# Optimization experiments

Hardware: AMD Instinct MI355X
Metric: run time of the kernel (lower is better)

## Reference

```python
import jax, jax.numpy as jnp
import numpy as np

N = 100000   # nodes
E = 1600000  # edges (before self loops)
B = 64       # graphs in batch
F_IN = 128
H1, C1 = 8, 8   # conv1: heads=8, per-head channels=8 -> concat out 64
H2, C2 = 1, 8   # conv2: heads=1, out=8, concat=False


def gat_conv(x, src, dst, W, att_src, att_dst, bias, H, C, concat, n_nodes):
    """PyG GATConv (shared src/dst weight, leaky_relu slope 0.2, segment softmax).
    src/dst already include self loops. x: [N, F], W: [F, H*C],
    att_src/att_dst: [1, H, C], bias: [H*C] or [C]."""
    xh = (x @ W).reshape(n_nodes, H, C)                      # [N, H, C]
    a_src = jnp.sum(xh * att_src, axis=-1)                   # [N, H]
    a_dst = jnp.sum(xh * att_dst, axis=-1)                   # [N, H]
    alpha = jax.nn.leaky_relu(a_src[src] + a_dst[dst], 0.2)  # [E', H]
    # numerically stable segment softmax over incoming edges of each dst node
    amax = jax.ops.segment_max(jax.lax.stop_gradient(alpha), dst, num_segments=n_nodes)
    ex = jnp.exp(alpha - amax[dst])
    denom = jax.ops.segment_sum(ex, dst, num_segments=n_nodes)
    alpha = ex / (denom[dst] + 1e-16)                        # [E', H]
    msg = xh[src] * alpha[..., None]                         # [E', H, C]
    out = jax.ops.segment_sum(msg, dst, num_segments=n_nodes)  # [N, H, C]
    out = out.reshape(n_nodes, H * C) if concat else out.mean(axis=1)
    return out + bias


def setup_inputs() -> dict:
    key = jax.random.key(0)
    ks = jax.random.split(key, 12)
    x = jax.random.normal(ks[0], (N, F_IN), dtype=jnp.float32)
    edge_index = jax.random.randint(ks[1], (2, E), 0, N, dtype=jnp.int32)
    batch = jnp.sort(jax.random.randint(ks[2], (N,), 0, B, dtype=jnp.int32))
    g = 0.1
    W1 = jax.random.normal(ks[3], (F_IN, H1 * C1), dtype=jnp.float32) * g
    a1_src = jax.random.normal(ks[4], (1, H1, C1), dtype=jnp.float32) * g
    a1_dst = jax.random.normal(ks[5], (1, H1, C1), dtype=jnp.float32) * g
    b1 = jnp.zeros((H1 * C1,), dtype=jnp.float32)
    W2 = jax.random.normal(ks[6], (H1 * C1, H2 * C2), dtype=jnp.float32) * g
    a2_src = jax.random.normal(ks[7], (1, H2, C2), dtype=jnp.float32) * g
    a2_dst = jax.random.normal(ks[8], (1, H2, C2), dtype=jnp.float32) * g
    b2 = jnp.zeros((C2,), dtype=jnp.float32)
    return {"x": x, "edge_index": edge_index, "batch": batch,
            "W1": W1, "a1_src": a1_src, "a1_dst": a1_dst, "b1": b1,
            "W2": W2, "a2_src": a2_src, "a2_dst": a2_dst, "b2": b2}


def reference(x, edge_index, batch, W1, a1_src, a1_dst, b1, W2, a2_src, a2_dst, b2):
    # add self loops (PyG GATConv default)
    loop = jnp.arange(N, dtype=edge_index.dtype)
    src = jnp.concatenate([edge_index[0], loop])
    dst = jnp.concatenate([edge_index[1], loop])
    # eval mode: dropouts are identity
    h = gat_conv(x, src, dst, W1, a1_src, a1_dst, b1, H1, C1, True, N)
    h = jax.nn.elu(h)
    h = gat_conv(h, src, dst, W2, a2_src, a2_dst, b2, H2, C2, False, N)
    # global mean pool over graphs
    sums = jax.ops.segment_sum(h, batch, num_segments=B)          # [B, C2]
    cnt = jax.ops.segment_sum(jnp.ones((N,), h.dtype), batch, num_segments=B)
    return sums / jnp.maximum(cnt, 1.0)[:, None]
```

## Files before the change

kernel.cpp:

```cpp
#include <hip/hip_runtime.h>
#include <hip/hip_bf16.h>

#define BIN_SHIFT 8
#define BIN_NODES 256
#define BIN_CAP   8192
#define EPT       16

typedef float v2f __attribute__((ext_vector_type(2)));

__device__ __forceinline__ float leaky02(float a) { return fmaxf(a, 0.2f * a); }
__device__ __forceinline__ unsigned short f2bf(float f) {
    __hip_bfloat16 h = __float2bfloat16(f);
    return *(unsigned short*)&h;
}
__device__ __forceinline__ float bflo(unsigned u) { return __uint_as_float(u << 16); }
__device__ __forceinline__ float bfhi(unsigned u) { return __uint_as_float(u & 0xffff0000u); }
__device__ __forceinline__ v2f bf2(unsigned u) {
    v2f r; r.x = __uint_as_float(u << 16); r.y = __uint_as_float(u & 0xffff0000u); return r;
}

__global__ __launch_bounds__(512) void gemm1_att_kernel(const float* __restrict__ x,
                                                        const float* __restrict__ W,
                                                        const float* __restrict__ a1s,
                                                        const float* __restrict__ a1d,
                                                        __hip_bfloat16* __restrict__ xh,
                                                        float* __restrict__ asrc,
                                                        float* __restrict__ adst, int N) {
    __shared__ float ws[128 * 64];
    __shared__ float xs[64][132];
    int tid = threadIdx.x;
    for (int i = tid; i < 2048; i += 512) ((float4*)ws)[i] = ((const float4*)W)[i];
    int row0 = blockIdx.x * 64;
    for (int i = tid; i < 64 * 32; i += 512) {
        int r = i >> 5, c4 = i & 31;
        int row = row0 + r;
        float4 v = make_float4(0.f, 0.f, 0.f, 0.f);
        if (row < N) v = ((const float4*)x)[row * 32 + c4];
        float* p = &xs[r][c4 * 4];
        p[0] = v.x; p[1] = v.y; p[2] = v.z; p[3] = v.w;
    }
    __syncthreads();
    int tc = tid & 15, tr = tid >> 4;
    float acc[2][4] = {};
#pragma unroll 4
    for (int k = 0; k < 128; ++k) {
        float a0 = xs[tr * 2][k];
        float a1 = xs[tr * 2 + 1][k];
        float4 b = *(const float4*)&ws[k * 64 + tc * 4];
        acc[0][0] += a0 * b.x; acc[0][1] += a0 * b.y; acc[0][2] += a0 * b.z; acc[0][3] += a0 * b.w;
        acc[1][0] += a1 * b.x; acc[1][1] += a1 * b.y; acc[1][2] += a1 * b.z; acc[1][3] += a1 * b.w;
    }
    float4 sv = ((const float4*)a1s)[tc];
    float4 dv = ((const float4*)a1d)[tc];
    int head = tc >> 1;
#pragma unroll
    for (int r = 0; r < 2; ++r) {
        int row = row0 + tr * 2 + r;
        if (row < N) {
            uint2 o;
            o.x = (unsigned)f2bf(acc[r][0]) | ((unsigned)f2bf(acc[r][1]) << 16);
            o.y = (unsigned)f2bf(acc[r][2]) | ((unsigned)f2bf(acc[r][3]) << 16);
            *(uint2*)(xh + (size_t)row * 64 + tc * 4) = o;
        }
        float sp = acc[r][0] * sv.x + acc[r][1] * sv.y + acc[r][2] * sv.z + acc[r][3] * sv.w;
        float dp = acc[r][0] * dv.x + acc[r][1] * dv.y + acc[r][2] * dv.z + acc[r][3] * dv.w;
        sp += __shfl_xor(sp, 1);
        dp += __shfl_xor(dp, 1);
        if (!(tc & 1) && row < N) {
            asrc[row * 8 + head] = sp;
            adst[row * 8 + head] = dp;
        }
    }
}

__global__ __launch_bounds__(256) void binB_kernel(const int* __restrict__ ei,
                                                   int* __restrict__ cur,
                                                   unsigned* __restrict__ binned,
                                                   int E, int Etot, int NB) {
    __shared__ int bcnt[512];
    int tid = threadIdx.x;
    for (int i = tid; i < 512; i += 256) bcnt[i] = 0;
    __syncthreads();
    long long base = (long long)blockIdx.x * 256 * EPT;
#pragma unroll 4
    for (int i = 0; i < EPT; ++i) {
        long long e = base + i * 256 + tid;
        if (e < Etot) {
            int dst = (e < E) ? ei[E + e] : (int)(e - E);
            atomicAdd(&bcnt[dst >> BIN_SHIFT], 1);
        }
    }
    __syncthreads();
    for (int b = tid; b < NB; b += 256) {
        int c = bcnt[b];
        bcnt[b] = c ? atomicAdd(&cur[b], c) : 0;
    }
    __syncthreads();
#pragma unroll 4
    for (int i = 0; i < EPT; ++i) {
        long long e = base + i * 256 + tid;
        if (e < Etot) {
            int src, dst;
            if (e < E) { src = ei[e]; dst = ei[E + e]; }
            else       { src = dst = (int)(e - E); }
            int bin = dst >> BIN_SHIFT;
            int p = atomicAdd(&bcnt[bin], 1);
            if (p < BIN_CAP)
                binned[(size_t)bin * BIN_CAP + p] = ((unsigned)(dst & (BIN_NODES - 1)) << 24) | (unsigned)src;
        }
    }
}

__global__ __launch_bounds__(256) void binC_kernel(const int* __restrict__ cur,
                                                   const unsigned* __restrict__ binned,
                                                   int* __restrict__ rowptr,
                                                   int* __restrict__ esrc,
                                                   int N, int Etot, int NB) {
    int bin = blockIdx.x;
    int tid = threadIdx.x;
    __shared__ int psum[256];
    __shared__ int sc[256];
    __shared__ int ndc[256];
    int s = 0;
    for (int i = tid; i < bin; i += 256) s += cur[i];
    psum[tid] = s;
    __syncthreads();
    for (int off = 128; off > 0; off >>= 1) {
        if (tid < off) psum[tid] += psum[tid + off];
        __syncthreads();
    }
    int bbase = psum[0];
    int cnt = cur[bin];
    ndc[tid] = 0;
    __syncthreads();
    const unsigned* bp = binned + (size_t)bin * BIN_CAP;
    for (int i = tid; i < cnt; i += 256)
        atomicAdd(&ndc[bp[i] >> 24], 1);
    __syncthreads();
    int v = ndc[tid];
    sc[tid] = v;
    __syncthreads();
    for (int off = 1; off < 256; off <<= 1) {
        int t = (tid >= off) ? sc[tid - off] : 0;
        __syncthreads();
        sc[tid] += t;
        __syncthreads();
    }
    int excl = sc[tid] - v;
    int node = bin * BIN_NODES + tid;
    if (node < N) rowptr[node] = bbase + excl;
    if (bin == NB - 1 && tid == 0) rowptr[N] = Etot;
    ndc[tid] = excl;
    __syncthreads();
    for (int i = tid; i < cnt; i += 256) {
        unsigned w = bp[i];
        int p = atomicAdd(&ndc[w >> 24], 1);
        esrc[bbase + p] = (int)(w & 0xFFFFFFu);
    }
}

__global__ __launch_bounds__(256) void agg1_kernel(const int* __restrict__ rowptr,
                                                   const int* __restrict__ esrc,
                                                   const float* __restrict__ asrc,
                                                   const float* __restrict__ adst,
                                                   const __hip_bfloat16* __restrict__ xh,
                                                   const float* __restrict__ b1,
                                                   __hip_bfloat16* __restrict__ h1, int N) {
    int node = blockIdx.x * 4 + (threadIdx.x >> 6);
    if (node >= N) return;
    int lane = threadIdx.x & 63;
    unsigned slot = (unsigned)(lane >> 3), h = (unsigned)(lane & 7);
    float adh = adst[(unsigned)node * 8u + h];
    unsigned start = (unsigned)rowptr[node];
    int len = rowptr[node + 1] - (int)start;
    const uint4* xh4 = (const uint4*)xh;
    float d = 0.f;
    v2f acc0 = {0.f, 0.f}, acc1 = {0.f, 0.f}, acc2 = {0.f, 0.f}, acc3 = {0.f, 0.f};
    for (int kb = 0; kb < len; kb += 32) {
        int k0 = kb + (int)slot;
        bool ok0 = k0 < len, ok1 = k0 + 8 < len, ok2 = k0 + 16 < len, ok3 = k0 + 24 < len;
        unsigned s0 = ok0 ? (unsigned)esrc[start + k0] : 0u;
        unsigned s1 = ok1 ? (unsigned)esrc[start + k0 + 8] : 0u;
        unsigned s2 = ok2 ? (unsigned)esrc[start + k0 + 16] : 0u;
        unsigned s3 = ok3 ? (unsigned)esrc[start + k0 + 24] : 0u;
        float a0 = ok0 ? asrc[s0 * 8u + h] : -1e30f;
        float a1 = ok1 ? asrc[s1 * 8u + h] : -1e30f;
        float a2 = ok2 ? asrc[s2 * 8u + h] : -1e30f;
        float a3 = ok3 ? asrc[s3 * 8u + h] : -1e30f;
        uint4 u0 = xh4[s0 * 8u + h];
        uint4 u1 = xh4[s1 * 8u + h];
        uint4 u2 = xh4[s2 * 8u + h];
        uint4 u3 = xh4[s3 * 8u + h];
        float p0 = __expf(leaky02(a0 + adh));
        float p1 = __expf(leaky02(a1 + adh));
        float p2 = __expf(leaky02(a2 + adh));
        float p3 = __expf(leaky02(a3 + adh));
        d += (p0 + p1) + (p2 + p3);
        acc0 += bf2(u0.x) * p0; acc1 += bf2(u0.y) * p0;
        acc2 += bf2(u0.z) * p0; acc3 += bf2(u0.w) * p0;
        acc0 += bf2(u1.x) * p1; acc1 += bf2(u1.y) * p1;
        acc2 += bf2(u1.z) * p1; acc3 += bf2(u1.w) * p1;
        acc0 += bf2(u2.x) * p2; acc1 += bf2(u2.y) * p2;
        acc2 += bf2(u2.z) * p2; acc3 += bf2(u2.w) * p2;
        acc0 += bf2(u3.x) * p3; acc1 += bf2(u3.y) * p3;
        acc2 += bf2(u3.z) * p3; acc3 += bf2(u3.w) * p3;
    }
#pragma unroll
    for (int off = 8; off < 64; off <<= 1) {
        d += __shfl_xor(d, off);
        acc0.x += __shfl_xor(acc0.x, off); acc0.y += __shfl_xor(acc0.y, off);
        acc1.x += __shfl_xor(acc1.x, off); acc1.y += __shfl_xor(acc1.y, off);
        acc2.x += __shfl_xor(acc2.x, off); acc2.y += __shfl_xor(acc2.y, off);
        acc3.x += __shfl_xor(acc3.x, off); acc3.y += __shfl_xor(acc3.y, off);
    }
    float vals[8] = {acc0.x, acc0.y, acc1.x, acc1.y, acc2.x, acc2.y, acc3.x, acc3.y};
    float hv = vals[0];
#pragma unroll
    for (int c = 1; c < 8; ++c) hv = ((int)slot == c) ? vals[c] : hv;
    int f = (int)(h * 8u + slot);
    hv = hv / (d + 1e-16f) + b1[f];
    hv = hv > 0.f ? hv : __expf(hv) - 1.0f;
    float hvp = __shfl(hv, ((lane & 7) << 3) | (lane >> 3));
    h1[(unsigned)node * 64u + (unsigned)lane] = __float2bfloat16(hvp);
}

__global__ __launch_bounds__(256) void gemm2h_kernel(const __hip_bfloat16* __restrict__ h1,
                                                     const float* __restrict__ W2,
                                                     const float* __restrict__ a2s,
                                                     const float* __restrict__ a2d,
                                                     __hip_bfloat16* __restrict__ xh2,
                                                     float* __restrict__ asrc2,
                                                     float* __restrict__ adst2, int N) {
    __shared__ float w2s[512];
    __shared__ float aa[16];
    int tid = threadIdx.x;
    for (int i = tid; i < 512; i += 256) w2s[i] = W2[i];
    if (tid < 8) aa[tid] = a2s[tid];
    else if (tid < 16) aa[tid] = a2d[tid - 8];
    __syncthreads();
    unsigned n = blockIdx.x * 256u + (unsigned)tid;
    if (n >= (unsigned)N) return;
    const uint4* hp = (const uint4*)h1 + n * 8u;
    float q[8] = {};
#pragma unroll
    for (int j = 0; j < 8; ++j) {
        uint4 u = hp[j];
        float hv[8] = {bflo(u.x), bfhi(u.x), bflo(u.y), bfhi(u.y),
                       bflo(u.z), bfhi(u.z), bflo(u.w), bfhi(u.w)};
#pragma unroll
        for (int e = 0; e < 8; ++e) {
            int f = j * 8 + e;
            float4 wa = *(const float4*)&w2s[f * 8];
            float4 wb = *(const float4*)&w2s[f * 8 + 4];
            q[0] += hv[e] * wa.x; q[1] += hv[e] * wa.y;
            q[2] += hv[e] * wa.z; q[3] += hv[e] * wa.w;
            q[4] += hv[e] * wb.x; q[5] += hv[e] * wb.y;
            q[6] += hv[e] * wb.z; q[7] += hv[e] * wb.w;
        }
    }
    uint4 o;
    o.x = (unsigned)f2bf(q[0]) | ((unsigned)f2bf(q[1]) << 16);
    o.y = (unsigned)f2bf(q[2]) | ((unsigned)f2bf(q[3]) << 16);
    o.z = (unsigned)f2bf(q[4]) | ((unsigned)f2bf(q[5]) << 16);
    o.w = (unsigned)f2bf(q[6]) | ((unsigned)f2bf(q[7]) << 16);
    *((uint4*)xh2 + n) = o;
    float s2 = 0.f, d2 = 0.f;
#pragma unroll
    for (int c = 0; c < 8; ++c) { s2 += q[c] * aa[c]; d2 += q[c] * aa[8 + c]; }
    asrc2[n] = s2;
    adst2[n] = d2;
}

__global__ __launch_bounds__(256) void agg2_pool_kernel(const int* __restrict__ rowptr,
                                                        const int* __restrict__ esrc,
                                                        const float* __restrict__ asrc2,
                                                        const float* __restrict__ adst2,
                                                        const __hip_bfloat16* __restrict__ xh2,
                                                        const float* __restrict__ b2,
                                                        const int* __restrict__ batch,
                                                        float* __restrict__ pool,
                                                        float* __restrict__ cnt, int N, int B) {
    __shared__ float ps[64 * 8];
    __shared__ float cs[64];
    int tid = threadIdx.x;
    for (int i = tid; i < 512; i += 256) ps[i] = 0.f;
    if (tid < 64) cs[tid] = 0.f;
    __syncthreads();
    int node = blockIdx.x * 32 + (tid >> 3);
    int slot = tid & 7;
    if (node < N) {
        float adh = adst2[node];
        unsigned start = (unsigned)rowptr[node];
        int len = rowptr[node + 1] - (int)start;
        const uint4* x4 = (const uint4*)xh2;
        float d = 0.f;
        v2f acc0 = {0.f, 0.f}, acc1 = {0.f, 0.f}, acc2 = {0.f, 0.f}, acc3 = {0.f, 0.f};
        for (int kb = 0; kb < len; kb += 32) {
            int k0 = kb + slot;
            bool ok0 = k0 < len, ok1 = k0 + 8 < len, ok2 = k0 + 16 < len, ok3 = k0 + 24 < len;
            unsigned s0 = ok0 ? (unsigned)esrc[start + k0] : 0u;
            unsigned s1 = ok1 ? (unsigned)esrc[start + k0 + 8] : 0u;
            unsigned s2 = ok2 ? (unsigned)esrc[start + k0 + 16] : 0u;
            unsigned s3 = ok3 ? (unsigned)esrc[start + k0 + 24] : 0u;
            float a0 = ok0 ? asrc2[s0] : -1e30f;
            float a1 = ok1 ? asrc2[s1] : -1e30f;
            float a2 = ok2 ? asrc2[s2] : -1e30f;
            float a3 = ok3 ? asrc2[s3] : -1e30f;
            uint4 u0 = x4[s0];
            uint4 u1 = x4[s1];
            uint4 u2 = x4[s2];
            uint4 u3 = x4[s3];
            float p0 = __expf(leaky02(a0 + adh));
            float p1 = __expf(leaky02(a1 + adh));
            float p2 = __expf(leaky02(a2 + adh));
            float p3 = __expf(leaky02(a3 + adh));
            d += (p0 + p1) + (p2 + p3);
            acc0 += bf2(u0.x) * p0; acc1 += bf2(u0.y) * p0;
            acc2 += bf2(u0.z) * p0; acc3 += bf2(u0.w) * p0;
            acc0 += bf2(u1.x) * p1; acc1 += bf2(u1.y) * p1;
            acc2 += bf2(u1.z) * p1; acc3 += bf2(u1.w) * p1;
            acc0 += bf2(u2.x) * p2; acc1 += bf2(u2.y) * p2;
            acc2 += bf2(u2.z) * p2; acc3 += bf2(u2.w) * p2;
            acc0 += bf2(u3.x) * p3; acc1 += bf2(u3.y) * p3;
            acc2 += bf2(u3.z) * p3; acc3 += bf2(u3.w) * p3;
        }
#pragma unroll
        for (int off = 1; off < 8; off <<= 1) {
            d += __shfl_xor(d, off);
            acc0.x += __shfl_xor(acc0.x, off); acc0.y += __shfl_xor(acc0.y, off);
            acc1.x += __shfl_xor(acc1.x, off); acc1.y += __shfl_xor(acc1.y, off);
            acc2.x += __shfl_xor(acc2.x, off); acc2.y += __shfl_xor(acc2.y, off);
            acc3.x += __shfl_xor(acc3.x, off); acc3.y += __shfl_xor(acc3.y, off);
        }
        float vals[8] = {acc0.x, acc0.y, acc1.x, acc1.y, acc2.x, acc2.y, acc3.x, acc3.y};
        float v = vals[0];
#pragma unroll
        for (int c = 1; c < 8; ++c) v = (slot == c) ? vals[c] : v;
        v = v / (d + 1e-16f) + b2[slot];
        int b = batch[node];
        atomicAdd(&ps[b * 8 + slot], v);
        if (slot == 0) atomicAdd(&cs[b], 1.0f);
    }
    __syncthreads();
    for (int i = tid; i < 512; i += 256)
        if (ps[i] != 0.f) atomicAdd(&pool[i], ps[i]);
    if (tid < 64 && cs[tid] != 0.f) atomicAdd(&cnt[tid], cs[tid]);
}

__global__ __launch_bounds__(256) void final_kernel(const float* __restrict__ pool,
                                                    const float* __restrict__ cnt,
                                                    float* __restrict__ out, int B) {
    int idx = blockIdx.x * 256 + threadIdx.x;
    if (idx >= B * 8) return;
    out[idx] = pool[idx] / fmaxf(cnt[idx >> 3], 1.0f);
}

extern "C" void kernel_launch(void* const* d_in, const int* in_sizes, int n_in,
                              void* d_out, int out_size, void* d_ws, size_t ws_size,
                              hipStream_t stream) {
    const float* x   = (const float*)d_in[0];
    const int*   ei  = (const int*)d_in[1];
    const int*   bat = (const int*)d_in[2];
    const float* W1  = (const float*)d_in[3];
    const float* a1s = (const float*)d_in[4];
    const float* a1d = (const float*)d_in[5];
    const float* b1  = (const float*)d_in[6];
    const float* W2  = (const float*)d_in[7];
    const float* a2s = (const float*)d_in[8];
    const float* a2d = (const float*)d_in[9];
    const float* b2  = (const float*)d_in[10];
    float* out = (float*)d_out;

    const int N = in_sizes[0] / 128;
    const int E = in_sizes[1] / 2;
    const int B = out_size / 8;
    const int Etot = E + N;
    const int NB = (N + BIN_NODES - 1) / BIN_NODES;

    float* wsp = (float*)d_ws;
    __hip_bfloat16* xh1 = (__hip_bfloat16*)wsp;
    float* asrc1  = wsp + (size_t)N * 32;
    float* adst1  = asrc1 + (size_t)N * 8;
    __hip_bfloat16* h1 = (__hip_bfloat16*)(adst1 + (size_t)N * 8);
    __hip_bfloat16* xh2 = (__hip_bfloat16*)(adst1 + (size_t)N * 40);
    float* asrc2  = adst1 + (size_t)N * 44;
    float* adst2  = asrc2 + (size_t)N;
    int*   rowptr = (int*)(adst2 + (size_t)N);
    int*   esrc   = rowptr + (size_t)N + 8;
    unsigned* binned = (unsigned*)(esrc + (size_t)Etot);
    int*   cur    = (int*)(binned + (size_t)NB * BIN_CAP);
    float* pool   = (float*)(cur + NB);
    float* cnt    = pool + (size_t)B * 8;
    size_t zbytes = ((size_t)NB + 9 * (size_t)B) * 4;
    hipMemsetAsync(cur, 0, zbytes, stream);

    gemm1_att_kernel<<<dim3((N + 63) / 64), dim3(512), 0, stream>>>(x, W1, a1s, a1d, xh1, asrc1, adst1, N);
    binB_kernel<<<dim3((Etot + 256 * EPT - 1) / (256 * EPT)), dim3(256), 0, stream>>>(ei, cur, binned, E, Etot, NB);
    binC_kernel<<<dim3(NB), dim3(256), 0, stream>>>(cur, binned, rowptr, esrc, N, Etot, NB);
    agg1_kernel<<<dim3((N + 3) / 4), dim3(256), 0, stream>>>(rowptr, esrc, asrc1, adst1, xh1, b1, h1, N);
    gemm2h_kernel<<<dim3((N + 255) / 256), dim3(256), 0, stream>>>(h1, W2, a2s, a2d, xh2, asrc2, adst2, N);
    agg2_pool_kernel<<<dim3((N + 31) / 32), dim3(256), 0, stream>>>(rowptr, esrc, asrc2, adst2,
                                                                    xh2, b2, bat, pool, cnt, N, B);
    final_kernel<<<dim3((B * 8 + 255) / 256), dim3(256), 0, stream>>>(pool, cnt, out, B);
}
```

Baseline: 180.5 us.

## Fuse edge binning into first GEMM kernel and halve rows per block

The separate edge-binning kernel is merged into the layer-1 GEMM/attention kernel. Each block now computes 32 rows (one row per thread group) and then bins a contiguous slice of the edge list into per-destination-node bins using shared-memory counters. The goal is to drop one kernel launch and overlap the memory-bound binning with the compute of the GEMM. In exchange there are twice as many blocks, each reloading the 32 KB W tile, and only about 513 edges per block, which may raise global atomic traffic on the bin cursors.

After: 217.6 us. +20.6%, slower.

```diff
diff --git a/kernel.cpp b/kernel.cpp
--- a/kernel.cpp
+++ b/kernel.cpp
@@ -4,7 +4,6 @@
 #define BIN_SHIFT 8
 #define BIN_NODES 256
 #define BIN_CAP   8192
-#define EPT       16
 
 typedef float v2f __attribute__((ext_vector_type(2)));
 
@@ -19,19 +18,25 @@
     v2f r; r.x = __uint_as_float(u << 16); r.y = __uint_as_float(u & 0xffff0000u); return r;
 }
 
-__global__ __launch_bounds__(512) void gemm1_att_kernel(const float* __restrict__ x,
+__global__ __launch_bounds__(512) void gemm1_bin_kernel(const float* __restrict__ x,
                                                         const float* __restrict__ W,
                                                         const float* __restrict__ a1s,
                                                         const float* __restrict__ a1d,
+                                                        const int* __restrict__ ei,
                                                         __hip_bfloat16* __restrict__ xh,
                                                         float* __restrict__ asrc,
-                                                        float* __restrict__ adst, int N) {
+                                                        float* __restrict__ adst,
+                                                        int* __restrict__ cur,
+                                                        unsigned* __restrict__ binned,
+                                                        int N, int E, int Etot, int NB) {
     __shared__ float ws[128 * 64];
-    __shared__ float xs[64][132];
+    __shared__ float xs[32][132];
+    __shared__ int bcnt[512];
     int tid = threadIdx.x;
+    for (int i = tid; i < 512; i += 512) bcnt[i] = 0;
     for (int i = tid; i < 2048; i += 512) ((float4*)ws)[i] = ((const float4*)W)[i];
-    int row0 = blockIdx.x * 64;
-    for (int i = tid; i < 64 * 32; i += 512) {
+    int row0 = blockIdx.x * 32;
+    for (int i = tid; i < 32 * 32; i += 512) {
         int r = i >> 5, c4 = i & 31;
         int row = row0 + r;
         float4 v = make_float4(0.f, 0.f, 0.f, 0.f);
@@ -41,73 +46,53 @@
     }
     __syncthreads();
     int tc = tid & 15, tr = tid >> 4;
-    float acc[2][4] = {};
+    float acc[4] = {};
 #pragma unroll 4
     for (int k = 0; k < 128; ++k) {
-        float a0 = xs[tr * 2][k];
-        float a1 = xs[tr * 2 + 1][k];
+        float a0 = xs[tr][k];
         float4 b = *(const float4*)&ws[k * 64 + tc * 4];
-        acc[0][0] += a0 * b.x; acc[0][1] += a0 * b.y; acc[0][2] += a0 * b.z; acc[0][3] += a0 * b.w;
-        acc[1][0] += a1 * b.x; acc[1][1] += a1 * b.y; acc[1][2] += a1 * b.z; acc[1][3] += a1 * b.w;
+        acc[0] += a0 * b.x; acc[1] += a0 * b.y; acc[2] += a0 * b.z; acc[3] += a0 * b.w;
+    }
+    int row = row0 + tr;
+    if (row < N) {
+        uint2 o;
+        o.x = (unsigned)f2bf(acc[0]) | ((unsigned)f2bf(acc[1]) << 16);
+        o.y = (unsigned)f2bf(acc[2]) | ((unsigned)f2bf(acc[3]) << 16);
+        *(uint2*)(xh + (size_t)row * 64 + tc * 4) = o;
     }
     float4 sv = ((const float4*)a1s)[tc];
     float4 dv = ((const float4*)a1d)[tc];
     int head = tc >> 1;
-#pragma unroll
-    for (int r = 0; r < 2; ++r) {
-        int row = row0 + tr * 2 + r;
-        if (row < N) {
-            uint2 o;
-            o.x = (unsigned)f2bf(acc[r][0]) | ((unsigned)f2bf(acc[r][1]) << 16);
-            o.y = (unsigned)f2bf(acc[r][2]) | ((unsigned)f2bf(acc[r][3]) << 16);
-            *(uint2*)(xh + (size_t)row * 64 + tc * 4) = o;
-        }
-        float sp = acc[r][0] * sv.x + acc[r][1] * sv.y + acc[r][2] * sv.z + acc[r][3] * sv.w;
-        float dp = acc[r][0] * dv.x + acc[r][1] * dv.y + acc[r][2] * dv.z + acc[r][3] * dv.w;
-        sp += __shfl_xor(sp, 1);
-        dp += __shfl_xor(dp, 1);
-        if (!(tc & 1) && row < N) {
-            asrc[row * 8 + head] = sp;
-            adst[row * 8 + head] = dp;
-        }
-    }
-}
-
-__global__ __launch_bounds__(256) void binB_kernel(const int* __restrict__ ei,
-                                                   int* __restrict__ cur,
-                                                   unsigned* __restrict__ binned,
-                                                   int E, int Etot, int NB) {
-    __shared__ int bcnt[512];
-    int tid = threadIdx.x;
-    for (int i = tid; i < 512; i += 256) bcnt[i] = 0;
-    __syncthreads();
-    long long base = (long long)blockIdx.x * 256 * EPT;
-#pragma unroll 4
-    for (int i = 0; i < EPT; ++i) {
-        long long e = base + i * 256 + tid;
-        if (e < Etot) {
-            int dst = (e < E) ? ei[E + e] : (int)(e - E);
-            atomicAdd(&bcnt[dst >> BIN_SHIFT], 1);
-        }
-    }
-    __syncthreads();
-    for (int b = tid; b < NB; b += 256) {
+    float sp = acc[0] * sv.x + acc[1] * sv.y + acc[2] * sv.z + acc[3] * sv.w;
+    float dp = acc[0] * dv.x + acc[1] * dv.y + acc[2] * dv.z + acc[3] * dv.w;
+    sp += __shfl_xor(sp, 1);
+    dp += __shfl_xor(dp, 1);
+    if (!(tc & 1) && row < N) {
+        asrc[row * 8 + head] = sp;
+        adst[row * 8 + head] = dp;
+    }
+    int nblk = gridDim.x;
+    long long per = ((long long)Etot + nblk - 1) / nblk;
+    long long e0 = (long long)blockIdx.x * per;
+    long long e1 = e0 + per; if (e1 > Etot) e1 = Etot;
+    for (long long e = e0 + tid; e < e1; e += 512) {
+        int dst = (e < E) ? ei[E + e] : (int)(e - E);
+        atomicAdd(&bcnt[dst >> BIN_SHIFT], 1);
+    }
+    __syncthreads();
+    for (int b = tid; b < NB; b += 512) {
         int c = bcnt[b];
         bcnt[b] = c ? atomicAdd(&cur[b], c) : 0;
     }
     __syncthreads();
-#pragma unroll 4
-    for (int i = 0; i < EPT; ++i) {
-        long long e = base + i * 256 + tid;
-        if (e < Etot) {
-            int src, dst;
-            if (e < E) { src = ei[e]; dst = ei[E + e]; }
-            else       { src = dst = (int)(e - E); }
-            int bin = dst >> BIN_SHIFT;
-            int p = atomicAdd(&bcnt[bin], 1);
-            if (p < BIN_CAP)
-                binned[(size_t)bin * BIN_CAP + p] = ((unsigned)(dst & (BIN_NODES - 1)) << 24) | (unsigned)src;
-        }
+    for (long long e = e0 + tid; e < e1; e += 512) {
+        int src, dst;
+        if (e < E) { src = ei[e]; dst = ei[E + e]; }
+        else       { src = dst = (int)(e - E); }
+        int bin = dst >> BIN_SHIFT;
+        int p = atomicAdd(&bcnt[bin], 1);
+        if (p < BIN_CAP)
+            binned[(size_t)bin * BIN_CAP + p] = ((unsigned)(dst & (BIN_NODES - 1)) << 24) | (unsigned)src;
     }
 }
 
@@ -394,8 +379,9 @@
     size_t zbytes = ((size_t)NB + 9 * (size_t)B) * 4;
     hipMemsetAsync(cur, 0, zbytes, stream);
 
-    gemm1_att_kernel<<<dim3((N + 63) / 64), dim3(512), 0, stream>>>(x, W1, a1s, a1d, xh1, asrc1, adst1, N);
-    binB_kernel<<<dim3((Etot + 256 * EPT - 1) / (256 * EPT)), dim3(256), 0, stream>>>(ei, cur, binned, E, Etot, NB);
+    gemm1_bin_kernel<<<dim3((N + 31) / 32), dim3(512), 0, stream>>>(x, W1, a1s, a1d, ei,
+                                                                    xh1, asrc1, adst1,
+                                                                    cur, binned, N, E, Etot, NB);
     binC_kernel<<<dim3(NB), dim3(256), 0, stream>>>(cur, binned, rowptr, esrc, N, Etot, NB);
     agg1_kernel<<<dim3((N + 3) / 4), dim3(256), 0, stream>>>(rowptr, esrc, asrc1, adst1, xh1, b1, h1, N);
     gemm2h_kernel<<<dim3((N + 255) / 256), dim3(256), 0, stream>>>(h1, W2, a2s, a2d, xh2, asrc2, adst2, N);
```

## Fuse edge binning into GEMM1 launch and split agg1 heads across two waves

Applied to the files above, without the earlier changes.

Merges the binB edge-binning kernel into the first GEMM kernel as extra 512-thread blocks, so binning and the layer-1 projection run concurrently in a single launch. Separately, agg1 now uses two wavefronts per node, each covering four heads with 16 edge slots per wave, and writes a packed uint4 of eight bf16 outputs per head instead of a lane-transposed shuffle store. The goal is to remove a launch boundary, overlap two independent phases, and raise parallelism in the gather. In exchange, every edge's src index and asrc value is read twice (once per wave), and the GEMM blocks share an oversized shared-memory footprint with the binning blocks.

Result: slower. 201.6 us (+11.7%).

```diff
diff --git a/kernel.cpp b/kernel.cpp
--- a/kernel.cpp
+++ b/kernel.cpp
@@ -19,18 +19,57 @@
     v2f r; r.x = __uint_as_float(u << 16); r.y = __uint_as_float(u & 0xffff0000u); return r;
 }
 
-__global__ __launch_bounds__(512) void gemm1_att_kernel(const float* __restrict__ x,
-                                                        const float* __restrict__ W,
-                                                        const float* __restrict__ a1s,
-                                                        const float* __restrict__ a1d,
-                                                        __hip_bfloat16* __restrict__ xh,
-                                                        float* __restrict__ asrc,
-                                                        float* __restrict__ adst, int N) {
+__global__ __launch_bounds__(512) void k1_kernel(const float* __restrict__ x,
+                                                 const float* __restrict__ W,
+                                                 const float* __restrict__ a1s,
+                                                 const float* __restrict__ a1d,
+                                                 const int* __restrict__ ei,
+                                                 __hip_bfloat16* __restrict__ xh,
+                                                 float* __restrict__ asrc,
+                                                 float* __restrict__ adst,
+                                                 int* __restrict__ cur,
+                                                 unsigned* __restrict__ binned,
+                                                 int N, int E, int Etot, int NB, int NBB) {
     __shared__ float ws[128 * 64];
     __shared__ float xs[64][132];
+    __shared__ int bcnt[512];
     int tid = threadIdx.x;
+    if (blockIdx.x < NBB) {
+        bcnt[tid] = 0;
+        __syncthreads();
+        long long base = (long long)blockIdx.x * 512 * EPT;
+#pragma unroll 4
+        for (int i = 0; i < EPT; ++i) {
+            long long e = base + i * 512 + tid;
+            if (e < Etot) {
+                int dst = (e < E) ? ei[E + e] : (int)(e - E);
+                atomicAdd(&bcnt[dst >> BIN_SHIFT], 1);
+            }
+        }
+        __syncthreads();
+        for (int b = tid; b < NB; b += 512) {
+            int c = bcnt[b];
+            bcnt[b] = c ? atomicAdd(&cur[b], c) : 0;
+        }
+        __syncthreads();
+#pragma unroll 4
+        for (int i = 0; i < EPT; ++i) {
+            long long e = base + i * 512 + tid;
+            if (e < Etot) {
+                int src, dst;
+                if (e < E) { src = ei[e]; dst = ei[E + e]; }
+                else       { src = dst = (int)(e - E); }
+                int bin = dst >> BIN_SHIFT;
+                int p = atomicAdd(&bcnt[bin], 1);
+                if (p < BIN_CAP)
+                    binned[(size_t)bin * BIN_CAP + p] = ((unsigned)(dst & (BIN_NODES - 1)) << 24) | (unsigned)src;
+            }
+        }
+        return;
+    }
+    int gb = blockIdx.x - NBB;
     for (int i = tid; i < 2048; i += 512) ((float4*)ws)[i] = ((const float4*)W)[i];
-    int row0 = blockIdx.x * 64;
+    int row0 = gb * 64;
     for (int i = tid; i < 64 * 32; i += 512) {
         int r = i >> 5, c4 = i & 31;
         int row = row0 + r;
@@ -69,44 +108,6 @@
         if (!(tc & 1) && row < N) {
             asrc[row * 8 + head] = sp;
             adst[row * 8 + head] = dp;
-        }
-    }
-}
-
-__global__ __launch_bounds__(256) void binB_kernel(const int* __restrict__ ei,
-                                                   int* __restrict__ cur,
-                                                   unsigned* __restrict__ binned,
-                                                   int E, int Etot, int NB) {
-    __shared__ int bcnt[512];
-    int tid = threadIdx.x;
-    for (int i = tid; i < 512; i += 256) bcnt[i] = 0;
-    __syncthreads();
-    long long base = (long long)blockIdx.x * 256 * EPT;
-#pragma unroll 4
-    for (int i = 0; i < EPT; ++i) {
-        long long e = base + i * 256 + tid;
-        if (e < Etot) {
-            int dst = (e < E) ? ei[E + e] : (int)(e - E);
-            atomicAdd(&bcnt[dst >> BIN_SHIFT], 1);
-        }
-    }
-    __syncthreads();
-    for (int b = tid; b < NB; b += 256) {
-        int c = bcnt[b];
-        bcnt[b] = c ? atomicAdd(&cur[b], c) : 0;
-    }
-    __syncthreads();
-#pragma unroll 4
-    for (int i = 0; i < EPT; ++i) {
-        long long e = base + i * 256 + tid;
-        if (e < Etot) {
-            int src, dst;
-            if (e < E) { src = ei[e]; dst = ei[E + e]; }
-            else       { src = dst = (int)(e - E); }
-            int bin = dst >> BIN_SHIFT;
-            int p = atomicAdd(&bcnt[bin], 1);
-            if (p < BIN_CAP)
-                binned[(size_t)bin * BIN_CAP + p] = ((unsigned)(dst & (BIN_NODES - 1)) << 24) | (unsigned)src;
         }
     }
 }
@@ -166,62 +167,64 @@
                                                    const __hip_bfloat16* __restrict__ xh,
                                                    const float* __restrict__ b1,
                                                    __hip_bfloat16* __restrict__ h1, int N) {
-    int node = blockIdx.x * 4 + (threadIdx.x >> 6);
-    if (node >= N) return;
+    int wid = blockIdx.x * 4 + (threadIdx.x >> 6);
+    if (wid >= 2 * N) return;
+    int pass = (wid >= N) ? 1 : 0;
+    int node = wid - pass * N;
     int lane = threadIdx.x & 63;
-    unsigned slot = (unsigned)(lane >> 3), h = (unsigned)(lane & 7);
-    float adh = adst[(unsigned)node * 8u + h];
+    unsigned slot = (unsigned)(lane >> 2), h = (unsigned)(lane & 3);
+    unsigned H = (unsigned)(pass * 4) + h;
+    float adh = adst[(unsigned)node * 8u + H];
     unsigned start = (unsigned)rowptr[node];
     int len = rowptr[node + 1] - (int)start;
     const uint4* xh4 = (const uint4*)xh;
     float d = 0.f;
     v2f acc0 = {0.f, 0.f}, acc1 = {0.f, 0.f}, acc2 = {0.f, 0.f}, acc3 = {0.f, 0.f};
     for (int kb = 0; kb < len; kb += 32) {
-        int k0 = kb + (int)slot;
-        bool ok0 = k0 < len, ok1 = k0 + 8 < len, ok2 = k0 + 16 < len, ok3 = k0 + 24 < len;
+        int k0 = kb + (int)slot, k1 = k0 + 16;
+        bool ok0 = k0 < len, ok1 = k1 < len;
         unsigned s0 = ok0 ? (unsigned)esrc[start + k0] : 0u;
-        unsigned s1 = ok1 ? (unsigned)esrc[start + k0 + 8] : 0u;
-        unsigned s2 = ok2 ? (unsigned)esrc[start + k0 + 16] : 0u;
-        unsigned s3 = ok3 ? (unsigned)esrc[start + k0 + 24] : 0u;
-        float a0 = ok0 ? asrc[s0 * 8u + h] : -1e30f;
-        float a1 = ok1 ? asrc[s1 * 8u + h] : -1e30f;
-        float a2 = ok2 ? asrc[s2 * 8u + h] : -1e30f;
-        float a3 = ok3 ? asrc[s3 * 8u + h] : -1e30f;
-        uint4 u0 = xh4[s0 * 8u + h];
-        uint4 u1 = xh4[s1 * 8u + h];
-        uint4 u2 = xh4[s2 * 8u + h];
-        uint4 u3 = xh4[s3 * 8u + h];
+        unsigned s1 = ok1 ? (unsigned)esrc[start + k1] : 0u;
+        float a0 = ok0 ? asrc[s0 * 8u + H] : -1e30f;
+        float a1 = ok1 ? asrc[s1 * 8u + H] : -1e30f;
+        uint4 u0 = xh4[s0 * 8u + H];
+        uint4 u1 = xh4[s1 * 8u + H];
         float p0 = __expf(leaky02(a0 + adh));
         float p1 = __expf(leaky02(a1 + adh));
-        float p2 = __expf(leaky02(a2 + adh));
-        float p3 = __expf(leaky02(a3 + adh));
-        d += (p0 + p1) + (p2 + p3);
+        d += p0 + p1;
         acc0 += bf2(u0.x) * p0; acc1 += bf2(u0.y) * p0;
         acc2 += bf2(u0.z) * p0; acc3 += bf2(u0.w) * p0;
         acc0 += bf2(u1.x) * p1; acc1 += bf2(u1.y) * p1;
         acc2 += bf2(u1.z) * p1; acc3 += bf2(u1.w) * p1;
-        acc0 += bf2(u2.x) * p2; acc1 += bf2(u2.y) * p2;
-        acc2 += bf2(u2.z) * p2; acc3 += bf2(u2.w) * p2;
-        acc0 += bf2(u3.x) * p3; acc1 += bf2(u3.y) * p3;
-        acc2 += bf2(u3.z) * p3; acc3 += bf2(u3.w) * p3;
-    }
-#pragma unroll
-    for (int off = 8; off < 64; off <<= 1) {
+    }
+#pragma unroll
+    for (int off = 4; off < 64; off <<= 1) {
         d += __shfl_xor(d, off);
         acc0.x += __shfl_xor(acc0.x, off); acc0.y += __shfl_xor(acc0.y, off);
         acc1.x += __shfl_xor(acc1.x, off); acc1.y += __shfl_xor(acc1.y, off);
         acc2.x += __shfl_xor(acc2.x, off); acc2.y += __shfl_xor(acc2.y, off);
         acc3.x += __shfl_xor(acc3.x, off); acc3.y += __shfl_xor(acc3.y, off);
     }
-    float vals[8] = {acc0.x, acc0.y, acc1.x, acc1.y, acc2.x, acc2.y, acc3.x, acc3.y};
-    float hv = vals[0];
-#pragma unroll
-    for (int c = 1; c < 8; ++c) hv = ((int)slot == c) ? vals[c] : hv;
-    int f = (int)(h * 8u + slot);
-    hv = hv / (d + 1e-16f) + b1[f];
-    hv = hv > 0.f ? hv : __expf(hv) - 1.0f;
-    float hvp = __shfl(hv, ((lane & 7) << 3) | (lane >> 3));
-    h1[(unsigned)node * 64u + (unsigned)lane] = __float2bfloat16(hvp);
+    if (slot == 0) {
+        float inv = 1.0f / (d + 1e-16f);
+        const float4* bp4 = (const float4*)(b1 + H * 8u);
+        float4 bA = bp4[0], bB = bp4[1];
+        float vals[8] = {acc0.x, acc0.y, acc1.x, acc1.y, acc2.x, acc2.y, acc3.x, acc3.y};
+        float bb[8] = {bA.x, bA.y, bA.z, bA.w, bB.x, bB.y, bB.z, bB.w};
+        unsigned short o16[8];
+#pragma unroll
+        for (int c = 0; c < 8; ++c) {
+            float v = vals[c] * inv + bb[c];
+            v = v > 0.f ? v : __expf(v) - 1.0f;
+            o16[c] = f2bf(v);
+        }
+        uint4 o;
+        o.x = (unsigned)o16[0] | ((unsigned)o16[1] << 16);
+        o.y = (unsigned)o16[2] | ((unsigned)o16[3] << 16);
+        o.z = (unsigned)o16[4] | ((unsigned)o16[5] << 16);
+        o.w = (unsigned)o16[6] | ((unsigned)o16[7] << 16);
+        *((uint4*)h1 + (size_t)node * 8u + H) = o;
+    }
 }
 
 __global__ __launch_bounds__(256) void gemm2h_kernel(const __hip_bfloat16* __restrict__ h1,
@@ -376,6 +379,8 @@
     const int B = out_size / 8;
     const int Etot = E + N;
     const int NB = (N + BIN_NODES - 1) / BIN_NODES;
+    const int NBB = (Etot + 512 * EPT - 1) / (512 * EPT);
+    const int NG = (N + 63) / 64;
 
     float* wsp = (float*)d_ws;
     __hip_bfloat16* xh1 = (__hip_bfloat16*)wsp;
@@ -394,10 +399,12 @@
     size_t zbytes = ((size_t)NB + 9 * (size_t)B) * 4;
     hipMemsetAsync(cur, 0, zbytes, stream);
 
-    gemm1_att_kernel<<<dim3((N + 63) / 64), dim3(512), 0, stream>>>(x, W1, a1s, a1d, xh1, asrc1, adst1, N);
-    binB_kernel<<<dim3((Etot + 256 * EPT - 1) / (256 * EPT)), dim3(256), 0, stream>>>(ei, cur, binned, E, Etot, NB);
+    k1_kernel<<<dim3(NBB + NG), dim3(512), 0, stream>>>(x, W1, a1s, a1d, ei,
+                                                        xh1, asrc1, adst1,
+                                                        cur, binned, N, E, Etot, NB, NBB);
     binC_kernel<<<dim3(NB), dim3(256), 0, stream>>>(cur, binned, rowptr, esrc, N, Etot, NB);
-    agg1_kernel<<<dim3((N + 3) / 4), dim3(256), 0, stream>>>(rowptr, esrc, asrc1, adst1, xh1, b1, h1, N);
+    agg1_kernel<<<dim3((2 * N + 3) / 4), dim3(256), 0, stream>>>(rowptr, esrc, asrc1, adst1,
+                                                                 xh1, b1, h1, N);
     gemm2h_kernel<<<dim3((N + 255) / 256), dim3(256), 0, stream>>>(h1, W2, a2s, a2d, xh2, asrc2, adst2, N);
     agg2_pool_kernel<<<dim3((N + 31) / 32), dim3(256), 0, stream>>>(rowptr, esrc, asrc2, adst2,
                                                                     xh2, b2, bat, pool, cnt, N, B);
```

## Fuse edge binning with gemm1 and fold gemm2 into layer-1 aggregation

Applied to the files above, without the earlier changes.

The edge binning pass and the first GEMM now run as one launch, with blocks split by index into binning blocks and GEMM blocks, so the two independent stages can overlap on the device. The second-layer projection and its attention dot products are computed inside the layer-1 aggregation kernel through wavefront shuffle reductions, which removes the h1 intermediate buffer and its write and read. The costs are a 48-step shuffle reduction per node and the large GEMM shared-memory allocation also applying to binning blocks, which may limit their occupancy.

Result: no change. 183.4 us (+1.6%).

```diff
diff --git a/kernel.cpp b/kernel.cpp
--- a/kernel.cpp
+++ b/kernel.cpp
@@ -13,24 +13,61 @@
     __hip_bfloat16 h = __float2bfloat16(f);
     return *(unsigned short*)&h;
 }
-__device__ __forceinline__ float bflo(unsigned u) { return __uint_as_float(u << 16); }
-__device__ __forceinline__ float bfhi(unsigned u) { return __uint_as_float(u & 0xffff0000u); }
 __device__ __forceinline__ v2f bf2(unsigned u) {
     v2f r; r.x = __uint_as_float(u << 16); r.y = __uint_as_float(u & 0xffff0000u); return r;
 }
 
-__global__ __launch_bounds__(512) void gemm1_att_kernel(const float* __restrict__ x,
-                                                        const float* __restrict__ W,
-                                                        const float* __restrict__ a1s,
-                                                        const float* __restrict__ a1d,
-                                                        __hip_bfloat16* __restrict__ xh,
-                                                        float* __restrict__ asrc,
-                                                        float* __restrict__ adst, int N) {
+__global__ __launch_bounds__(512) void k1_kernel(const float* __restrict__ x,
+                                                 const float* __restrict__ W,
+                                                 const float* __restrict__ a1s,
+                                                 const float* __restrict__ a1d,
+                                                 const int* __restrict__ ei,
+                                                 __hip_bfloat16* __restrict__ xh,
+                                                 float* __restrict__ asrc,
+                                                 float* __restrict__ adst,
+                                                 int* __restrict__ cur,
+                                                 unsigned* __restrict__ binned,
+                                                 int N, int E, int Etot, int NB, int NBB) {
     __shared__ float ws[128 * 64];
     __shared__ float xs[64][132];
+    __shared__ int bcnt[512];
     int tid = threadIdx.x;
+    if (blockIdx.x < NBB) {
+        bcnt[tid] = 0;
+        __syncthreads();
+        long long base = (long long)blockIdx.x * 512 * EPT;
+#pragma unroll 4
+        for (int i = 0; i < EPT; ++i) {
+            long long e = base + i * 512 + tid;
+            if (e < Etot) {
+                int dst = (e < E) ? ei[E + e] : (int)(e - E);
+                atomicAdd(&bcnt[dst >> BIN_SHIFT], 1);
+            }
+        }
+        __syncthreads();
+        for (int b = tid; b < NB; b += 512) {
+            int c = bcnt[b];
+            bcnt[b] = c ? atomicAdd(&cur[b], c) : 0;
+        }
+        __syncthreads();
+#pragma unroll 4
+        for (int i = 0; i < EPT; ++i) {
+            long long e = base + i * 512 + tid;
+            if (e < Etot) {
+                int src, dst;
+                if (e < E) { src = ei[e]; dst = ei[E + e]; }
+                else       { src = dst = (int)(e - E); }
+                int bin = dst >> BIN_SHIFT;
+                int p = atomicAdd(&bcnt[bin], 1);
+                if (p < BIN_CAP)
+                    binned[(size_t)bin * BIN_CAP + p] = ((unsigned)(dst & (BIN_NODES - 1)) << 24) | (unsigned)src;
+            }
+        }
+        return;
+    }
+    int gb = blockIdx.x - NBB;
     for (int i = tid; i < 2048; i += 512) ((float4*)ws)[i] = ((const float4*)W)[i];
-    int row0 = blockIdx.x * 64;
+    int row0 = gb * 64;
     for (int i = tid; i < 64 * 32; i += 512) {
         int r = i >> 5, c4 = i & 31;
         int row = row0 + r;
@@ -69,44 +106,6 @@
         if (!(tc & 1) && row < N) {
             asrc[row * 8 + head] = sp;
             adst[row * 8 + head] = dp;
-        }
-    }
-}
-
-__global__ __launch_bounds__(256) void binB_kernel(const int* __restrict__ ei,
-                                                   int* __restrict__ cur,
-                                                   unsigned* __restrict__ binned,
-                                                   int E, int Etot, int NB) {
-    __shared__ int bcnt[512];
-    int tid = threadIdx.x;
-    for (int i = tid; i < 512; i += 256) bcnt[i] = 0;
-    __syncthreads();
-    long long base = (long long)blockIdx.x * 256 * EPT;
-#pragma unroll 4
-    for (int i = 0; i < EPT; ++i) {
-        long long e = base + i * 256 + tid;
-        if (e < Etot) {
-            int dst = (e < E) ? ei[E + e] : (int)(e - E);
-            atomicAdd(&bcnt[dst >> BIN_SHIFT], 1);
-        }
-    }
-    __syncthreads();
-    for (int b = tid; b < NB; b += 256) {
-        int c = bcnt[b];
-        bcnt[b] = c ? atomicAdd(&cur[b], c) : 0;
-    }
-    __syncthreads();
-#pragma unroll 4
-    for (int i = 0; i < EPT; ++i) {
-        long long e = base + i * 256 + tid;
-        if (e < Etot) {
-            int src, dst;
-            if (e < E) { src = ei[e]; dst = ei[E + e]; }
-            else       { src = dst = (int)(e - E); }
-            int bin = dst >> BIN_SHIFT;
-            int p = atomicAdd(&bcnt[bin], 1);
-            if (p < BIN_CAP)
-                binned[(size_t)bin * BIN_CAP + p] = ((unsigned)(dst & (BIN_NODES - 1)) << 24) | (unsigned)src;
         }
     }
 }
@@ -159,13 +158,18 @@
     }
 }
 
-__global__ __launch_bounds__(256) void agg1_kernel(const int* __restrict__ rowptr,
-                                                   const int* __restrict__ esrc,
-                                                   const float* __restrict__ asrc,
-                                                   const float* __restrict__ adst,
-                                                   const __hip_bfloat16* __restrict__ xh,
-                                                   const float* __restrict__ b1,
-                                                   __hip_bfloat16* __restrict__ h1, int N) {
+__global__ __launch_bounds__(256) void agg1_fused_kernel(const int* __restrict__ rowptr,
+                                                         const int* __restrict__ esrc,
+                                                         const float* __restrict__ asrc,
+                                                         const float* __restrict__ adst,
+                                                         const __hip_bfloat16* __restrict__ xh,
+                                                         const float* __restrict__ b1,
+                                                         const float* __restrict__ W2,
+                                                         const float* __restrict__ a2s,
+                                                         const float* __restrict__ a2d,
+                                                         __hip_bfloat16* __restrict__ xh2,
+                                                         float* __restrict__ asrc2,
+                                                         float* __restrict__ adst2, int N) {
     int node = blockIdx.x * 4 + (threadIdx.x >> 6);
     if (node >= N) return;
     int lane = threadIdx.x & 63;
@@ -213,62 +217,35 @@
         acc2.x += __shfl_xor(acc2.x, off); acc2.y += __shfl_xor(acc2.y, off);
         acc3.x += __shfl_xor(acc3.x, off); acc3.y += __shfl_xor(acc3.y, off);
     }
+    float inv = 1.0f / (d + 1e-16f);
     float vals[8] = {acc0.x, acc0.y, acc1.x, acc1.y, acc2.x, acc2.y, acc3.x, acc3.y};
     float hv = vals[0];
 #pragma unroll
     for (int c = 1; c < 8; ++c) hv = ((int)slot == c) ? vals[c] : hv;
     int f = (int)(h * 8u + slot);
-    hv = hv / (d + 1e-16f) + b1[f];
+    hv = hv * inv + b1[f];
     hv = hv > 0.f ? hv : __expf(hv) - 1.0f;
-    float hvp = __shfl(hv, ((lane & 7) << 3) | (lane >> 3));
-    h1[(unsigned)node * 64u + (unsigned)lane] = __float2bfloat16(hvp);
-}
-
-__global__ __launch_bounds__(256) void gemm2h_kernel(const __hip_bfloat16* __restrict__ h1,
-                                                     const float* __restrict__ W2,
-                                                     const float* __restrict__ a2s,
-                                                     const float* __restrict__ a2d,
-                                                     __hip_bfloat16* __restrict__ xh2,
-                                                     float* __restrict__ asrc2,
-                                                     float* __restrict__ adst2, int N) {
-    __shared__ float w2s[512];
-    __shared__ float aa[16];
-    int tid = threadIdx.x;
-    for (int i = tid; i < 512; i += 256) w2s[i] = W2[i];
-    if (tid < 8) aa[tid] = a2s[tid];
-    else if (tid < 16) aa[tid] = a2d[tid - 8];
-    __syncthreads();
-    unsigned n = blockIdx.x * 256u + (unsigned)tid;
-    if (n >= (unsigned)N) return;
-    const uint4* hp = (const uint4*)h1 + n * 8u;
-    float q[8] = {};
-#pragma unroll
-    for (int j = 0; j < 8; ++j) {
-        uint4 u = hp[j];
-        float hv[8] = {bflo(u.x), bfhi(u.x), bflo(u.y), bfhi(u.y),
-                       bflo(u.z), bfhi(u.z), bflo(u.w), bfhi(u.w)};
-#pragma unroll
-        for (int e = 0; e < 8; ++e) {
-            int f = j * 8 + e;
-            float4 wa = *(const float4*)&w2s[f * 8];
-            float4 wb = *(const float4*)&w2s[f * 8 + 4];
-            q[0] += hv[e] * wa.x; q[1] += hv[e] * wa.y;
-            q[2] += hv[e] * wa.z; q[3] += hv[e] * wa.w;
-            q[4] += hv[e] * wb.x; q[5] += hv[e] * wb.y;
-            q[6] += hv[e] * wb.z; q[7] += hv[e] * wb.w;
-        }
-    }
-    uint4 o;
-    o.x = (unsigned)f2bf(q[0]) | ((unsigned)f2bf(q[1]) << 16);
-    o.y = (unsigned)f2bf(q[2]) | ((unsigned)f2bf(q[3]) << 16);
-    o.z = (unsigned)f2bf(q[4]) | ((unsigned)f2bf(q[5]) << 16);
-    o.w = (unsigned)f2bf(q[6]) | ((unsigned)f2bf(q[7]) << 16);
-    *((uint4*)xh2 + n) = o;
-    float s2 = 0.f, d2 = 0.f;
-#pragma unroll
-    for (int c = 0; c < 8; ++c) { s2 += q[c] * aa[c]; d2 += q[c] * aa[8 + c]; }
-    asrc2[n] = s2;
-    adst2[n] = d2;
+    const float4* wp = (const float4*)(W2 + f * 8);
+    float4 w0 = wp[0], w1 = wp[1];
+    float q[8] = {hv * w0.x, hv * w0.y, hv * w0.z, hv * w0.w,
+                  hv * w1.x, hv * w1.y, hv * w1.z, hv * w1.w};
+#pragma unroll
+    for (int off = 1; off < 64; off <<= 1)
+#pragma unroll
+        for (int c = 0; c < 8; ++c) q[c] += __shfl_xor(q[c], off);
+    if (lane == 0) {
+        uint4 o;
+        o.x = (unsigned)f2bf(q[0]) | ((unsigned)f2bf(q[1]) << 16);
+        o.y = (unsigned)f2bf(q[2]) | ((unsigned)f2bf(q[3]) << 16);
+        o.z = (unsigned)f2bf(q[4]) | ((unsigned)f2bf(q[5]) << 16);
+        o.w = (unsigned)f2bf(q[6]) | ((unsigned)f2bf(q[7]) << 16);
+        *((uint4*)xh2 + node) = o;
+        float s2 = 0.f, d2 = 0.f;
+#pragma unroll
+        for (int c = 0; c < 8; ++c) { s2 += q[c] * a2s[c]; d2 += q[c] * a2d[c]; }
+        asrc2[node] = s2;
+        adst2[node] = d2;
+    }
 }
 
 __global__ __launch_bounds__(256) void agg2_pool_kernel(const int* __restrict__ rowptr,
@@ -376,14 +353,15 @@
     const int B = out_size / 8;
     const int Etot = E + N;
     const int NB = (N + BIN_NODES - 1) / BIN_NODES;
+    const int NBB = (Etot + 512 * EPT - 1) / (512 * EPT);
+    const int NG = (N + 63) / 64;
 
     float* wsp = (float*)d_ws;
     __hip_bfloat16* xh1 = (__hip_bfloat16*)wsp;
     float* asrc1  = wsp + (size_t)N * 32;
     float* adst1  = asrc1 + (size_t)N * 8;
-    __hip_bfloat16* h1 = (__hip_bfloat16*)(adst1 + (size_t)N * 8);
-    __hip_bfloat16* xh2 = (__hip_bfloat16*)(adst1 + (size_t)N * 40);
-    float* asrc2  = adst1 + (size_t)N * 44;
+    __hip_bfloat16* xh2 = (__hip_bfloat16*)(adst1 + (size_t)N * 8);
+    float* asrc2  = adst1 + (size_t)N * 12;
     float* adst2  = asrc2 + (size_t)N;
     int*   rowptr = (int*)(adst2 + (size_t)N);
     int*   esrc   = rowptr + (size_t)N + 8;
@@ -394,11 +372,13 @@
     size_t zbytes = ((size_t)NB + 9 * (size_t)B) * 4;
     hipMemsetAsync(cur, 0, zbytes, stream);
 
-    gemm1_att_kernel<<<dim3((N + 63) / 64), dim3(512), 0, stream>>>(x, W1, a1s, a1d, xh1, asrc1, adst1, N);
-    binB_kernel<<<dim3((Etot + 256 * EPT - 1) / (256 * EPT)), dim3(256), 0, stream>>>(ei, cur, binned, E, Etot, NB);
+    k1_kernel<<<dim3(NBB + NG), dim3(512), 0, stream>>>(x, W1, a1s, a1d, ei,
+                                                        xh1, asrc1, adst1,
+                                                        cur, binned, N, E, Etot, NB, NBB);
     binC_kernel<<<dim3(NB), dim3(256), 0, stream>>>(cur, binned, rowptr, esrc, N, Etot, NB);
-    agg1_kernel<<<dim3((N + 3) / 4), dim3(256), 0, stream>>>(rowptr, esrc, asrc1, adst1, xh1, b1, h1, N);
-    gemm2h_kernel<<<dim3((N + 255) / 256), dim3(256), 0, stream>>>(h1, W2, a2s, a2d, xh2, asrc2, adst2, N);
+    agg1_fused_kernel<<<dim3((N + 3) / 4), dim3(256), 0, stream>>>(rowptr, esrc, asrc1, adst1,
+                                                                   xh1, b1, W2, a2s, a2d,
+                                                                   xh2, asrc2, adst2, N);
     agg2_pool_kernel<<<dim3((N + 31) / 32), dim3(256), 0, stream>>>(rowptr, esrc, asrc2, adst2,
                                                                     xh2, b2, bat, pool, cnt, N, B);
     final_kernel<<<dim3((B * 8 + 255) / 256), dim3(256), 0, stream>>>(pool, cnt, out, B);
```
